# Performance work log

Hardware: AMD Instinct MI355X
Metric: run time of the kernel (lower is better)

The kernel has to match this reference:

```python
import jax, jax.numpy as jnp
import numpy as np

CONF_THRESH = 0.9  # init kwarg confidence_thresh


def setup_inputs() -> dict:
    key = jax.random.key(0)
    k1, _ = jax.random.split(key)
    T, B, C = 2048, 64, 512
    pred = jax.random.normal(k1, (T, B, C), dtype=jnp.float32)
    mask = jnp.ones((T, B, 1), dtype=jnp.float32)
    return {"pred": pred, "mask": mask}


def reference(pred, mask):
    # pred: [T, B, C] raw scores; mask: [T, B, 1]
    C = pred.shape[-1]
    p = jax.nn.softmax(pred * mask, axis=2).reshape(-1, C)  # [N, C] probabilities
    # torch: np.where(p > thresh) selects (row, class) pairs, then
    # NLLLoss(strong_preds, classes) = mean over pairs of -p[row, class].
    sel = p > CONF_THRESH                      # [N, C] bool, selection mask
    cnt = jnp.sum(sel)                         # number of selected (row, class) pairs
    total = jnp.sum(jnp.where(sel, p, jnp.zeros((), p.dtype)))
    loss = -total / jnp.maximum(cnt, 1).astype(p.dtype)
    # if nothing passes the threshold, the original returns 0
    return jnp.where(cnt > 0, loss, jnp.zeros((), p.dtype))
```

## Files before the change

kernel.cpp:

```cpp
#include <hip/hip_runtime.h>


#define NCLS 512
#define THRESH 0.9f

__global__ void pl_init(float* ws) {
    ws[0] = 0.0f;
    ((unsigned int*)ws)[1] = 0u;
}

__global__ __launch_bounds__(256) void pl_main(const float* __restrict__ pred,
                                               const float* __restrict__ mask,
                                               float* __restrict__ ws,
                                               int N) {
    const int lane = threadIdx.x & 63;
    const int wid  = threadIdx.x >> 6;

    __shared__ float sTotal;
    __shared__ unsigned int sCnt;
    if (threadIdx.x == 0) { sTotal = 0.0f; sCnt = 0u; }
    __syncthreads();

    float wTotal = 0.0f;
    unsigned int wCnt = 0u;

    const long long rstride = (long long)gridDim.x * 4;
    for (long long row = (long long)blockIdx.x * 4 + wid; row < N; row += rstride) {
        const float mval = mask[row];
        const float4* rp = (const float4*)(pred + row * NCLS);
        float4 a = rp[lane];
        float4 b = rp[lane + 64];
        float x0 = a.x * mval, x1 = a.y * mval, x2 = a.z * mval, x3 = a.w * mval;
        float x4 = b.x * mval, x5 = b.y * mval, x6 = b.z * mval, x7 = b.w * mval;

        float mx = fmaxf(fmaxf(fmaxf(x0, x1), fmaxf(x2, x3)),
                         fmaxf(fmaxf(x4, x5), fmaxf(x6, x7)));
        #pragma unroll
        for (int off = 1; off < 64; off <<= 1)
            mx = fmaxf(mx, __shfl_xor(mx, off));

        float s = __expf(x0 - mx) + __expf(x1 - mx) + __expf(x2 - mx) + __expf(x3 - mx)
                + __expf(x4 - mx) + __expf(x5 - mx) + __expf(x6 - mx) + __expf(x7 - mx);
        #pragma unroll
        for (int off = 1; off < 64; off <<= 1)
            s += __shfl_xor(s, off);

        float pmax = 1.0f / s;
        if (lane == 0 && pmax > THRESH) { wTotal += pmax; wCnt += 1u; }
    }

    if (lane == 0 && wCnt > 0u) {
        atomicAdd(&sTotal, wTotal);
        atomicAdd(&sCnt, wCnt);
    }
    __syncthreads();
    if (threadIdx.x == 0 && sCnt > 0u) {
        atomicAdd(&ws[0], sTotal);
        atomicAdd((unsigned int*)ws + 1, sCnt);
    }
}

__global__ void pl_final(const float* __restrict__ ws, float* __restrict__ out) {
    unsigned int cnt = ((const unsigned int*)ws)[1];
    out[0] = (cnt > 0u) ? (-ws[0] / (float)cnt) : 0.0f;
}

extern "C" void kernel_launch(void* const* d_in, const int* in_sizes, int n_in,
                              void* d_out, int out_size, void* d_ws, size_t ws_size,
                              hipStream_t stream) {
    const float* pred = (const float*)d_in[0];
    const float* mask = (const float*)d_in[1];
    float* out = (float*)d_out;
    float* ws  = (float*)d_ws;

    const int N = in_sizes[0] / NCLS;

    pl_init<<<1, 1, 0, stream>>>(ws);

    const int blocks = 2048;
    pl_main<<<blocks, 256, 0, stream>>>(pred, mask, ws, N);

    pl_final<<<1, 1, 0, stream>>>(ws, out);
}
```

Measured before the change: 50.82 us.

## Replace atomics with per-block partials, unroll row loop by two, drop init kernel

New measurement: 49.30 us. 1.03x faster.

```diff
diff --git a/kernel.cpp b/kernel.cpp
--- a/kernel.cpp
+++ b/kernel.cpp
@@ -3,66 +3,99 @@
 
 #define NCLS 512
 #define THRESH 0.9f
+#define NBLOCKS 2048
 
-__global__ void pl_init(float* ws) {
-    ws[0] = 0.0f;
-    ((unsigned int*)ws)[1] = 0u;
+__device__ __forceinline__ void row_reduce(float4 a, float4 b, float mval,
+                                           float& wTotal, float& wCnt) {
+    float x0 = a.x * mval, x1 = a.y * mval, x2 = a.z * mval, x3 = a.w * mval;
+    float x4 = b.x * mval, x5 = b.y * mval, x6 = b.z * mval, x7 = b.w * mval;
+
+    float mx = fmaxf(fmaxf(fmaxf(x0, x1), fmaxf(x2, x3)),
+                     fmaxf(fmaxf(x4, x5), fmaxf(x6, x7)));
+    #pragma unroll
+    for (int off = 1; off < 64; off <<= 1)
+        mx = fmaxf(mx, __shfl_xor(mx, off));
+
+    float s = __expf(x0 - mx) + __expf(x1 - mx) + __expf(x2 - mx) + __expf(x3 - mx)
+            + __expf(x4 - mx) + __expf(x5 - mx) + __expf(x6 - mx) + __expf(x7 - mx);
+    #pragma unroll
+    for (int off = 1; off < 64; off <<= 1)
+        s += __shfl_xor(s, off);
+
+    float pmax = 1.0f / s;
+    if (pmax > THRESH) { wTotal += pmax; wCnt += 1.0f; }
 }
 
 __global__ __launch_bounds__(256) void pl_main(const float* __restrict__ pred,
                                                const float* __restrict__ mask,
-                                               float* __restrict__ ws,
+                                               float2* __restrict__ partial,
                                                int N) {
     const int lane = threadIdx.x & 63;
     const int wid  = threadIdx.x >> 6;
 
-    __shared__ float sTotal;
-    __shared__ unsigned int sCnt;
-    if (threadIdx.x == 0) { sTotal = 0.0f; sCnt = 0u; }
-    __syncthreads();
-
     float wTotal = 0.0f;
-    unsigned int wCnt = 0u;
+    float wCnt   = 0.0f;
 
     const long long rstride = (long long)gridDim.x * 4;
-    for (long long row = (long long)blockIdx.x * 4 + wid; row < N; row += rstride) {
-        const float mval = mask[row];
-        const float4* rp = (const float4*)(pred + row * NCLS);
-        float4 a = rp[lane];
-        float4 b = rp[lane + 64];
-        float x0 = a.x * mval, x1 = a.y * mval, x2 = a.z * mval, x3 = a.w * mval;
-        float x4 = b.x * mval, x5 = b.y * mval, x6 = b.z * mval, x7 = b.w * mval;
+    long long row = (long long)blockIdx.x * 4 + wid;
 
-        float mx = fmaxf(fmaxf(fmaxf(x0, x1), fmaxf(x2, x3)),
-                         fmaxf(fmaxf(x4, x5), fmaxf(x6, x7)));
-        #pragma unroll
-        for (int off = 1; off < 64; off <<= 1)
-            mx = fmaxf(mx, __shfl_xor(mx, off));
-
-        float s = __expf(x0 - mx) + __expf(x1 - mx) + __expf(x2 - mx) + __expf(x3 - mx)
-                + __expf(x4 - mx) + __expf(x5 - mx) + __expf(x6 - mx) + __expf(x7 - mx);
-        #pragma unroll
-        for (int off = 1; off < 64; off <<= 1)
-            s += __shfl_xor(s, off);
-
-        float pmax = 1.0f / s;
-        if (lane == 0 && pmax > THRESH) { wTotal += pmax; wCnt += 1u; }
+    for (; row + rstride < (long long)N; row += 2 * rstride) {
+        const long long r2 = row + rstride;
+        const float m1 = mask[row];
+        const float m2 = mask[r2];
+        const float4* rp1 = (const float4*)(pred + row * NCLS);
+        const float4* rp2 = (const float4*)(pred + r2 * NCLS);
+        float4 a1 = rp1[lane];
+        float4 b1 = rp1[lane + 64];
+        float4 a2 = rp2[lane];
+        float4 b2 = rp2[lane + 64];
+        row_reduce(a1, b1, m1, wTotal, wCnt);
+        row_reduce(a2, b2, m2, wTotal, wCnt);
+    }
+    for (; row < (long long)N; row += rstride) {
+        const float m1 = mask[row];
+        const float4* rp1 = (const float4*)(pred + row * NCLS);
+        float4 a1 = rp1[lane];
+        float4 b1 = rp1[lane + 64];
+        row_reduce(a1, b1, m1, wTotal, wCnt);
     }
 
-    if (lane == 0 && wCnt > 0u) {
-        atomicAdd(&sTotal, wTotal);
-        atomicAdd(&sCnt, wCnt);
-    }
+    __shared__ float sT[4];
+    __shared__ float sC[4];
+    if (lane == 0) { sT[wid] = wTotal; sC[wid] = wCnt; }
     __syncthreads();
-    if (threadIdx.x == 0 && sCnt > 0u) {
-        atomicAdd(&ws[0], sTotal);
-        atomicAdd((unsigned int*)ws + 1, sCnt);
+    if (threadIdx.x == 0) {
+        float t = sT[0] + sT[1] + sT[2] + sT[3];
+        float c = sC[0] + sC[1] + sC[2] + sC[3];
+        partial[blockIdx.x] = make_float2(t, c);
     }
 }
 
-__global__ void pl_final(const float* __restrict__ ws, float* __restrict__ out) {
-    unsigned int cnt = ((const unsigned int*)ws)[1];
-    out[0] = (cnt > 0u) ? (-ws[0] / (float)cnt) : 0.0f;
+__global__ __launch_bounds__(256) void pl_final(const float2* __restrict__ partial,
+                                                int nb, float* __restrict__ out) {
+    const int lane = threadIdx.x & 63;
+    const int wid  = threadIdx.x >> 6;
+
+    float t = 0.0f, c = 0.0f;
+    for (int i = threadIdx.x; i < nb; i += 256) {
+        float2 p = partial[i];
+        t += p.x;
+        c += p.y;
+    }
+    #pragma unroll
+    for (int off = 1; off < 64; off <<= 1) {
+        t += __shfl_xor(t, off);
+        c += __shfl_xor(c, off);
+    }
+    __shared__ float sT[4];
+    __shared__ float sC[4];
+    if (lane == 0) { sT[wid] = t; sC[wid] = c; }
+    __syncthreads();
+    if (threadIdx.x == 0) {
+        float tt = sT[0] + sT[1] + sT[2] + sT[3];
+        float cc = sC[0] + sC[1] + sC[2] + sC[3];
+        out[0] = (cc > 0.0f) ? (-tt / cc) : 0.0f;
+    }
 }
 
 extern "C" void kernel_launch(void* const* d_in, const int* in_sizes, int n_in,
@@ -71,14 +104,10 @@
     const float* pred = (const float*)d_in[0];
     const float* mask = (const float*)d_in[1];
     float* out = (float*)d_out;
-    float* ws  = (float*)d_ws;
+    float2* partial = (float2*)d_ws;
 
     const int N = in_sizes[0] / NCLS;
 
-    pl_init<<<1, 1, 0, stream>>>(ws);
-
-    const int blocks = 2048;
-    pl_main<<<blocks, 256, 0, stream>>>(pred, mask, ws, N);
-
-    pl_final<<<1, 1, 0, stream>>>(ws, out);
+    pl_main<<<NBLOCKS, 256, 0, stream>>>(pred, mask, partial, N);
+    pl_final<<<1, 256, 0, stream>>>(partial, NBLOCKS, out);
 }
```
